# Performance work log

Measured on AMD Instinct MI355X. Metric: run time of the kernel, lower is better.

Reference implementation:

```python
import jax, jax.numpy as jnp
import numpy as np

D_MODEL = 1024
NUM_HEADS = 16
D_K = D_MODEL // NUM_HEADS
B, N = 2, 2048


def setup_inputs() -> dict:
    key = jax.random.key(0)
    ks = jax.random.split(key, 11)
    s = 1.0 / np.sqrt(D_MODEL)
    inp = {
        "query": jax.random.normal(ks[0], (B, N, D_MODEL), jnp.float32),
        "key": jax.random.normal(ks[1], (B, N, D_MODEL), jnp.float32),
        "value": jax.random.normal(ks[2], (B, N, D_MODEL), jnp.float32),
        "w_q": jax.random.normal(ks[3], (D_MODEL, D_MODEL), jnp.float32) * s,
        "b_q": jax.random.normal(ks[4], (D_MODEL,), jnp.float32) * s,
        "w_k": jax.random.normal(ks[5], (D_MODEL, D_MODEL), jnp.float32) * s,
        "b_k": jax.random.normal(ks[6], (D_MODEL,), jnp.float32) * s,
        "w_v": jax.random.normal(ks[7], (D_MODEL, D_MODEL), jnp.float32) * s,
        "b_v": jax.random.normal(ks[8], (D_MODEL,), jnp.float32) * s,
        "w_o": jax.random.normal(ks[9], (D_MODEL, D_MODEL), jnp.float32) * s,
        "b_o": jax.random.normal(ks[10], (D_MODEL,), jnp.float32) * s,
    }
    return inp


def reference(query, key, value, w_q, b_q, w_k, b_k, w_v, b_v, w_o, b_o):
    Bq, Nq, _ = query.shape
    # projections (torch Linear: x @ W.T + b)
    Q = (query @ w_q.T + b_q).reshape(Bq, Nq, NUM_HEADS, D_K).transpose(0, 2, 1, 3)
    K = (key @ w_k.T + b_k).reshape(Bq, -1, NUM_HEADS, D_K).transpose(0, 2, 1, 3)
    V = (value @ w_v.T + b_v).reshape(Bq, -1, NUM_HEADS, D_K).transpose(0, 2, 1, 3)
    scores = jnp.einsum("bhqd,bhkd->bhqk", Q, K) / np.sqrt(D_K).astype(np.float32)
    attn = jax.nn.softmax(scores, axis=-1)  # dropout p=0.0 -> identity
    ctx = jnp.einsum("bhqk,bhkd->bhqd", attn, V)
    ctx = ctx.transpose(0, 2, 1, 3).reshape(Bq, Nq, D_MODEL)
    return ctx @ w_o.T + b_o
```

## Files before the change

### kernel.cpp

```cpp
#include <hip/hip_runtime.h>
#include <math.h>

#define D_MODEL 1024
#define NUM_HEADS 16
#define DK 64
#define BATCH 2
#define NSEQ 2048
#define MROWS (BATCH * NSEQ)

typedef __attribute__((ext_vector_type(8))) short bf16x8;
typedef __attribute__((ext_vector_type(4))) short s16x4;
typedef __attribute__((ext_vector_type(4))) float f32x4;
typedef unsigned short u16;

static __device__ __forceinline__ u16 f2bf_rne(float x) {
    union { float f; unsigned u; } v; v.f = x;
    unsigned r = v.u + 0x7fffu + ((v.u >> 16) & 1u);
    return (u16)(r >> 16);
}
static __device__ __forceinline__ void split_bf16(float x, u16& hi, u16& lo) {
    union { float f; unsigned u; } v; v.f = x;
    unsigned hb = v.u & 0xffff0000u;
    hi = (u16)(hb >> 16);
    union { unsigned u; float f; } hv; hv.u = hb;
    lo = f2bf_rne(x - hv.f);
}

#define AS1 __attribute__((address_space(1)))
#define AS3 __attribute__((address_space(3)))
static __device__ __forceinline__ void gl_lds16(const void* g, void* l) {
    __builtin_amdgcn_global_load_lds((AS1 void*)(uintptr_t)g, (AS3 void*)l, 16, 0, 0);
}

struct SplitN { const float* src[4]; u16* h[4]; u16* l[4]; };
__global__ __launch_bounds__(256)
void split_multi(SplitN args, int n8)
{
    const int w = blockIdx.y;
    const int i = blockIdx.x * 256 + threadIdx.x;
    if (i >= n8) return;
    const float* src = args.src[w];
    float4 a = ((const float4*)src)[2 * i];
    float4 b = ((const float4*)src)[2 * i + 1];
    float x[8] = {a.x, a.y, a.z, a.w, b.x, b.y, b.z, b.w};
    u16 hh[8], ll[8];
#pragma unroll
    for (int j = 0; j < 8; ++j) split_bf16(x[j], hh[j], ll[j]);
    *(uint4*)(args.h[w] + 8 * (size_t)i) = *(uint4*)hh;
    *(uint4*)(args.l[w] + 8 * (size_t)i) = *(uint4*)ll;
}

#define GBM 128
#define GBN 64
#define GBK 64

struct GemmDesc {
    const u16 *Ah, *Al, *Wh, *Wl;
    const float* bias;
    float* outF;
    u16 *outH, *outL;
    float scale;
    int mode;
};
struct GemmBatch { GemmDesc d[3]; };

__global__ __launch_bounds__(256)
void gemm_mfma_batch(GemmBatch batch, int M, int N, int K)
{
    __shared__ u16 SM[2 * GBM * GBK + 2 * GBN * GBK];
    u16* As_h = SM;
    u16* As_l = SM + GBM * GBK;
    u16* Ws_h = SM + 2 * GBM * GBK;
    u16* Ws_l = SM + 2 * GBM * GBK + GBN * GBK;

    const GemmDesc d = batch.d[blockIdx.z];
    const int tid  = threadIdx.x;
    const int wv   = tid >> 6, lane = tid & 63;
    const int quad = lane >> 4, lcol = lane & 15;
    const int bm = blockIdx.x * GBM, bn = blockIdx.y * GBN;
    const int wm = (wv >> 1) * 64, wn = (wv & 1) * 32;
    const int sj = lane >> 3, sg = lane & 7;
    const int sgx8 = ((sg ^ sj) << 3);

    f32x4 acc[4][2];
#pragma unroll
    for (int i = 0; i < 4; ++i)
#pragma unroll
        for (int j = 0; j < 2; ++j) acc[i][j] = (f32x4){0.f, 0.f, 0.f, 0.f};

    for (int k0 = 0; k0 < K; k0 += GBK) {
        __syncthreads();
#pragma unroll
        for (int c = 0; c < 4; ++c) {
            const int r0 = wv * 32 + c * 8;
            gl_lds16(d.Ah + (size_t)(bm + r0 + sj) * K + k0 + sgx8, As_h + r0 * GBK);
            gl_lds16(d.Al + (size_t)(bm + r0 + sj) * K + k0 + sgx8, As_l + r0 * GBK);
        }
#pragma unroll
        for (int c = 0; c < 2; ++c) {
            const int r0 = wv * 16 + c * 8;
            gl_lds16(d.Wh + (size_t)(bn + r0 + sj) * K + k0 + sgx8, Ws_h + r0 * GBK);
            gl_lds16(d.Wl + (size_t)(bn + r0 + sj) * K + k0 + sgx8, Ws_l + r0 * GBK);
        }
        __syncthreads();

#pragma unroll
        for (int hf = 0; hf < 2; ++hf) {
            const int sl = ((((hf << 2) + quad) ^ (lcol & 7)) << 3);
            bf16x8 bh[2], bl[2];
#pragma unroll
            for (int j = 0; j < 2; ++j) {
                const int rn = wn + (j << 4) + lcol;
                bh[j] = *(const bf16x8*)(Ws_h + rn * GBK + sl);
                bl[j] = *(const bf16x8*)(Ws_l + rn * GBK + sl);
            }
#pragma unroll
            for (int i = 0; i < 4; ++i) {
                const int rm = wm + (i << 4) + lcol;
                bf16x8 ah = *(const bf16x8*)(As_h + rm * GBK + sl);
                bf16x8 al = *(const bf16x8*)(As_l + rm * GBK + sl);
#pragma unroll
                for (int j = 0; j < 2; ++j) {
                    acc[i][j] = __builtin_amdgcn_mfma_f32_16x16x32_bf16(ah, bh[j], acc[i][j], 0, 0, 0);
                    acc[i][j] = __builtin_amdgcn_mfma_f32_16x16x32_bf16(al, bh[j], acc[i][j], 0, 0, 0);
                    acc[i][j] = __builtin_amdgcn_mfma_f32_16x16x32_bf16(ah, bl[j], acc[i][j], 0, 0, 0);
                }
            }
        }
    }

    if (d.mode == 2) {
        const int TS = 136;
        u16* T = SM;
        __syncthreads();
#pragma unroll
        for (int j = 0; j < 2; ++j) {
            const int cl = wn + (j << 4) + lcol;
            const float bj = d.bias[bn + cl];
#pragma unroll
            for (int i = 0; i < 4; ++i) {
                const int r0 = wm + (i << 4) + quad * 4;
                u16 pk[4];
#pragma unroll
                for (int r = 0; r < 4; ++r) pk[r] = f2bf_rne(acc[i][j][r] + bj);
                *(ushort4*)(T + cl * TS + r0) = *(ushort4*)pk;
            }
        }
        __syncthreads();
        const int dd = tid >> 2, pt = tid & 3;
        const int bidx = bm >> 11, hh = bn >> 6;
        u16* dst = d.outH + ((size_t)(bidx * NUM_HEADS + hh) * DK + dd) * NSEQ
                 + (bm & (NSEQ - 1)) + pt * 32;
        const u16* src = T + dd * TS + pt * 32;
#pragma unroll
        for (int k = 0; k < 4; ++k)
            ((uint4*)dst)[k] = *(const uint4*)(src + 8 * k);
        return;
    }

#pragma unroll
    for (int j = 0; j < 2; ++j) {
        const int col = bn + wn + (j << 4) + lcol;
        const float bj = d.bias[col];
#pragma unroll
        for (int i = 0; i < 4; ++i) {
#pragma unroll
            for (int r = 0; r < 4; ++r) {
                const int row = bm + wm + (i << 4) + quad * 4 + r;
                const float v = (acc[i][j][r] + bj) * d.scale;
                const size_t o = (size_t)row * N + col;
                if (d.mode == 0) {
                    d.outF[o] = v;
                } else {
                    u16 hi, lo;
                    split_bf16(v, hi, lo);
                    d.outH[o] = hi;
                    d.outL[o] = lo;
                }
            }
        }
    }
}

__global__ __launch_bounds__(256)
void flash_attn(const u16* __restrict__ Qh_g, const u16* __restrict__ Ql_g,
                const u16* __restrict__ Kh_g, const u16* __restrict__ Kl_g,
                const u16* __restrict__ Vt_g,
                u16* __restrict__ Ch_g, u16* __restrict__ Cl_g)
{
    __shared__ __align__(16) u16 Ks_h[64][72], Ks_l[64][72];
    __shared__ __align__(16) u16 Vs[64][72];

    const int tid  = threadIdx.x;
    const int wv   = tid >> 6;
    const int lane = tid & 63;
    const int quad = lane >> 4;
    const int lcol = lane & 15;
    const int h    = blockIdx.x;
    const int q0   = blockIdx.y << 7;
    const int b    = blockIdx.z;
    const size_t hbase  = (size_t)b * NSEQ * D_MODEL + (size_t)h * DK;
    const size_t vtbase = (size_t)(b * NUM_HEADS + h) * DK * NSEQ;

    bf16x8 bQh[2][2], bQl[2][2];
#pragma unroll
    for (int s = 0; s < 2; ++s) {
        const u16* qh = Qh_g + hbase + (size_t)(q0 + wv * 32 + s * 16 + lcol) * D_MODEL;
        const u16* ql = Ql_g + hbase + (size_t)(q0 + wv * 32 + s * 16 + lcol) * D_MODEL;
#pragma unroll
        for (int c = 0; c < 2; ++c) {
            bQh[s][c] = *(const bf16x8*)(qh + c * 32 + quad * 8);
            bQl[s][c] = *(const bf16x8*)(ql + c * 32 + quad * 8);
        }
    }

    f32x4 Oacc[2][4];
#pragma unroll
    for (int s = 0; s < 2; ++s)
#pragma unroll
        for (int t = 0; t < 4; ++t) Oacc[s][t] = (f32x4){0.f, 0.f, 0.f, 0.f};
    float mrow[2] = {-INFINITY, -INFINITY};
    float lrow[2] = {0.f, 0.f};

    const int lr = tid >> 2;
    const int lc = (tid & 3) << 4;

    const int NT = NSEQ / 64;
    const u16* gKh = Kh_g + hbase + (size_t)lr * D_MODEL + lc;
    const u16* gKl = Kl_g + hbase + (size_t)lr * D_MODEL + lc;
    const u16* gV  = Vt_g + vtbase + (size_t)lr * NSEQ + lc;

    uint4 s0 = *(const uint4*)(gKh);
    uint4 s1 = *(const uint4*)(gKh + 8);
    uint4 s2 = *(const uint4*)(gKl);
    uint4 s3 = *(const uint4*)(gKl + 8);
    uint4 s4 = *(const uint4*)(gV);
    uint4 s5 = *(const uint4*)(gV + 8);

    for (int kt = 0; kt < NT; ++kt) {
        __syncthreads();
        *(uint4*)&Ks_h[lr][lc]     = s0;
        *(uint4*)&Ks_h[lr][lc + 8] = s1;
        *(uint4*)&Ks_l[lr][lc]     = s2;
        *(uint4*)&Ks_l[lr][lc + 8] = s3;
        *(uint4*)&Vs[lr][lc]       = s4;
        *(uint4*)&Vs[lr][lc + 8]   = s5;
        __syncthreads();
        if (kt + 1 < NT) {
            const size_t ko = (size_t)(kt + 1) << 6;
            s0 = *(const uint4*)(gKh + ko * D_MODEL);
            s1 = *(const uint4*)(gKh + ko * D_MODEL + 8);
            s2 = *(const uint4*)(gKl + ko * D_MODEL);
            s3 = *(const uint4*)(gKl + ko * D_MODEL + 8);
            s4 = *(const uint4*)(gV + ko);
            s5 = *(const uint4*)(gV + ko + 8);
        }

        f32x4 S[2][4];
        __builtin_amdgcn_s_setprio(1);
#pragma unroll
        for (int t = 0; t < 4; ++t) {
            bf16x8 aKh0 = *(const bf16x8*)&Ks_h[(t << 4) + lcol][quad * 8];
            bf16x8 aKh1 = *(const bf16x8*)&Ks_h[(t << 4) + lcol][32 + quad * 8];
            bf16x8 aKl0 = *(const bf16x8*)&Ks_l[(t << 4) + lcol][quad * 8];
            bf16x8 aKl1 = *(const bf16x8*)&Ks_l[(t << 4) + lcol][32 + quad * 8];
#pragma unroll
            for (int s = 0; s < 2; ++s) {
                f32x4 a = (f32x4){0.f, 0.f, 0.f, 0.f};
                a = __builtin_amdgcn_mfma_f32_16x16x32_bf16(aKh0, bQh[s][0], a, 0, 0, 0);
                a = __builtin_amdgcn_mfma_f32_16x16x32_bf16(aKh1, bQh[s][1], a, 0, 0, 0);
                a = __builtin_amdgcn_mfma_f32_16x16x32_bf16(aKl0, bQh[s][0], a, 0, 0, 0);
                a = __builtin_amdgcn_mfma_f32_16x16x32_bf16(aKl1, bQh[s][1], a, 0, 0, 0);
                a = __builtin_amdgcn_mfma_f32_16x16x32_bf16(aKh0, bQl[s][0], a, 0, 0, 0);
                a = __builtin_amdgcn_mfma_f32_16x16x32_bf16(aKh1, bQl[s][1], a, 0, 0, 0);
                S[s][t] = a;
            }
        }
        __builtin_amdgcn_s_setprio(0);

        bf16x8 pb[2][2];
#pragma unroll
        for (int s = 0; s < 2; ++s) {
            float m16 = -INFINITY;
#pragma unroll
            for (int t = 0; t < 4; ++t)
#pragma unroll
                for (int r = 0; r < 4; ++r) m16 = fmaxf(m16, S[s][t][r]);
            m16 = fmaxf(m16, __shfl_xor(m16, 16, 64));
            m16 = fmaxf(m16, __shfl_xor(m16, 32, 64));
            const float mn = fmaxf(mrow[s], m16);
            const float alpha = __expf(mrow[s] - mn);
            mrow[s] = mn;

            float p[4][4];
            float psum = 0.f;
#pragma unroll
            for (int t = 0; t < 4; ++t)
#pragma unroll
                for (int r = 0; r < 4; ++r) {
                    const float pv = __expf(S[s][t][r] - mn);
                    p[t][r] = pv;
                    psum += pv;
                }
            psum += __shfl_xor(psum, 16, 64);
            psum += __shfl_xor(psum, 32, 64);
            lrow[s] = alpha * lrow[s] + psum;

#pragma unroll
            for (int c = 0; c < 2; ++c) {
                bf16x8 v;
#pragma unroll
                for (int r = 0; r < 4; ++r) {
                    v[r]     = (short)f2bf_rne(p[2 * c][r]);
                    v[4 + r] = (short)f2bf_rne(p[2 * c + 1][r]);
                }
                pb[s][c] = v;
            }
#pragma unroll
            for (int t = 0; t < 4; ++t)
#pragma unroll
                for (int r = 0; r < 4; ++r) Oacc[s][t][r] *= alpha;
        }

        __builtin_amdgcn_s_setprio(1);
#pragma unroll
        for (int dt = 0; dt < 4; ++dt) {
            const u16* vr = &Vs[(dt << 4) + lcol][0];
#pragma unroll
            for (int c = 0; c < 2; ++c) {
                s16x4 alo = *(const s16x4*)(vr + c * 32 + quad * 4);
                s16x4 ahi = *(const s16x4*)(vr + c * 32 + 16 + quad * 4);
                bf16x8 aV;
#pragma unroll
                for (int r = 0; r < 4; ++r) { aV[r] = alo[r]; aV[4 + r] = ahi[r]; }
#pragma unroll
                for (int s = 0; s < 2; ++s)
                    Oacc[s][dt] = __builtin_amdgcn_mfma_f32_16x16x32_bf16(aV, pb[s][c], Oacc[s][dt], 0, 0, 0);
            }
        }
        __builtin_amdgcn_s_setprio(0);
    }

#pragma unroll
    for (int s = 0; s < 2; ++s) {
        const float inv = 1.f / lrow[s];
        const size_t base = hbase + (size_t)(q0 + wv * 32 + s * 16 + lcol) * D_MODEL;
#pragma unroll
        for (int dt = 0; dt < 4; ++dt) {
            u16 hv[4], lv[4];
#pragma unroll
            for (int r = 0; r < 4; ++r)
                split_bf16(Oacc[s][dt][r] * inv, hv[r], lv[r]);
            const size_t o = base + (dt << 4) + quad * 4;
            *(ushort4*)(Ch_g + o) = *(ushort4*)hv;
            *(ushort4*)(Cl_g + o) = *(ushort4*)lv;
        }
    }
}

extern "C" void kernel_launch(void* const* d_in, const int* in_sizes, int n_in,
                              void* d_out, int out_size, void* d_ws, size_t ws_size,
                              hipStream_t stream)
{
    const float* query = (const float*)d_in[0];
    const float* key_i = (const float*)d_in[1];
    const float* value = (const float*)d_in[2];
    const float* w_q   = (const float*)d_in[3];
    const float* b_q   = (const float*)d_in[4];
    const float* w_k   = (const float*)d_in[5];
    const float* b_k   = (const float*)d_in[6];
    const float* w_v   = (const float*)d_in[7];
    const float* b_v   = (const float*)d_in[8];
    const float* w_o   = (const float*)d_in[9];
    const float* b_o   = (const float*)d_in[10];
    float* out = (float*)d_out;

    const size_t WE = (size_t)D_MODEL * D_MODEL;
    const size_t AE = (size_t)MROWS * D_MODEL;

    u16* p = (u16*)d_ws;
    u16* Wqh = p;            u16* Wql = Wqh + WE;
    u16* Wkh = Wql + WE;     u16* Wkl = Wkh + WE;
    u16* Wvh = Wkl + WE;     u16* Wvl = Wvh + WE;
    u16* Woh = Wvl + WE;     u16* Wol = Woh + WE;
    u16* base = Wol + WE;

    SplitN ws4;
    ws4.src[0] = w_q; ws4.h[0] = Wqh; ws4.l[0] = Wql;
    ws4.src[1] = w_k; ws4.h[1] = Wkh; ws4.l[1] = Wkl;
    ws4.src[2] = w_v; ws4.h[2] = Wvh; ws4.l[2] = Wvl;
    ws4.src[3] = w_o; ws4.h[3] = Woh; ws4.l[3] = Wol;
    split_multi<<<dim3((unsigned)(WE / 8 / 256), 4), 256, 0, stream>>>(ws4, (int)(WE / 8));

    const float qscale = 0.125f;
    dim3 fgrid(NUM_HEADS, NSEQ / 128, BATCH);
    dim3 ggrid3(MROWS / GBM, D_MODEL / GBN, 3);
    dim3 ggrid1(MROWS / GBM, D_MODEL / GBN, 1);
    const int an8 = (int)(AE / 8);

    const size_t fused_bytes = 2 * (8 * WE + 11 * AE);
    if (ws_size >= fused_bytes) {
        u16* INqh = base;          u16* INql = INqh + AE;
        u16* INkh = INql + AE;     u16* INkl = INkh + AE;
        u16* INvh = INkl + AE;     u16* INvl = INvh + AE;
        u16* Qph  = INvl + AE;     u16* Qpl  = Qph + AE;
        u16* Kph  = Qpl + AE;      u16* Kpl  = Kph + AE;
        u16* VT   = Kpl + AE;
        u16* Ch   = INqh;          u16* Cl   = INql;

        SplitN as3;
        as3.src[0] = query; as3.h[0] = INqh; as3.l[0] = INql;
        as3.src[1] = key_i; as3.h[1] = INkh; as3.l[1] = INkl;
        as3.src[2] = value; as3.h[2] = INvh; as3.l[2] = INvl;
        as3.src[3] = query; as3.h[3] = INqh; as3.l[3] = INql;
        split_multi<<<dim3((unsigned)(AE / 8 / 256), 3), 256, 0, stream>>>(as3, an8);

        GemmBatch gb;
        gb.d[0] = {INqh, INql, Wqh, Wql, b_q, nullptr, Qph, Qpl, qscale, 1};
        gb.d[1] = {INkh, INkl, Wkh, Wkl, b_k, nullptr, Kph, Kpl, 1.0f,   1};
        gb.d[2] = {INvh, INvl, Wvh, Wvl, b_v, nullptr, VT,  nullptr, 1.0f, 2};
        gemm_mfma_batch<<<ggrid3, 256, 0, stream>>>(gb, MROWS, D_MODEL, D_MODEL);

        flash_attn<<<fgrid, 256, 0, stream>>>(Qph, Qpl, Kph, Kpl, VT, Ch, Cl);

        GemmBatch go;
        go.d[0] = {Ch, Cl, Woh, Wol, b_o, out, nullptr, nullptr, 1.0f, 0};
        gemm_mfma_batch<<<ggrid1, 256, 0, stream>>>(go, MROWS, D_MODEL, D_MODEL);
    } else {
        u16* INh = base;           u16* INl = INh + AE;
        u16* Qph = INl + AE;       u16* Qpl = Qph + AE;
        u16* Kph = Qpl + AE;       u16* Kpl = Kph + AE;
        u16* VT  = Kpl + AE;
        u16* Ch  = INh;            u16* Cl  = INl;

        SplitN s1;
        s1.src[0] = query; s1.h[0] = INh; s1.l[0] = INl;
        s1.src[1] = s1.src[2] = s1.src[3] = query;
        s1.h[1] = s1.h[2] = s1.h[3] = INh; s1.l[1] = s1.l[2] = s1.l[3] = INl;

        GemmBatch g;
        s1.src[0] = query;
        split_multi<<<dim3((unsigned)(AE / 8 / 256), 1), 256, 0, stream>>>(s1, an8);
        g.d[0] = {INh, INl, Wqh, Wql, b_q, nullptr, Qph, Qpl, qscale, 1};
        gemm_mfma_batch<<<ggrid1, 256, 0, stream>>>(g, MROWS, D_MODEL, D_MODEL);

        s1.src[0] = key_i;
        split_multi<<<dim3((unsigned)(AE / 8 / 256), 1), 256, 0, stream>>>(s1, an8);
        g.d[0] = {INh, INl, Wkh, Wkl, b_k, nullptr, Kph, Kpl, 1.0f, 1};
        gemm_mfma_batch<<<ggrid1, 256, 0, stream>>>(g, MROWS, D_MODEL, D_MODEL);

        s1.src[0] = value;
        split_multi<<<dim3((unsigned)(AE / 8 / 256), 1), 256, 0, stream>>>(s1, an8);
        g.d[0] = {INh, INl, Wvh, Wvl, b_v, nullptr, VT, nullptr, 1.0f, 2};
        gemm_mfma_batch<<<ggrid1, 256, 0, stream>>>(g, MROWS, D_MODEL, D_MODEL);

        flash_attn<<<fgrid, 256, 0, stream>>>(Qph, Qpl, Kph, Kpl, VT, Ch, Cl);

        g.d[0] = {Ch, Cl, Woh, Wol, b_o, out, nullptr, nullptr, 1.0f, 0};
        gemm_mfma_batch<<<ggrid1, 256, 0, stream>>>(g, MROWS, D_MODEL, D_MODEL);
    }
}
```

Baseline: 332.1 us.

## Halve flash-attention query tile to 64 rows and use packed bf16 conversion

Each flash-attention block now handles 64 query rows instead of 128, with each wave owning one 16-row slice, so the grid doubles to 1024 blocks and register pressure drops. The software round-to-nearest bf16 conversion of probabilities is replaced with the hardware v_cvt_pk_bf16_f32 instruction, and the row max is reduced via a three-input max pattern. The cost is that every K/V tile is now loaded twice as often per query row, doubling K/V traffic, and each block does less MFMA work to hide each barrier and load.

```diff
diff --git a/kernel.cpp b/kernel.cpp
--- a/kernel.cpp
+++ b/kernel.cpp
@@ -24,6 +24,14 @@
     hi = (u16)(hb >> 16);
     union { unsigned u; float f; } hv; hv.u = hb;
     lo = f2bf_rne(x - hv.f);
+}
+static __device__ __forceinline__ unsigned cvt_pk_bf16(float a, float b) {
+    unsigned w;
+    asm("v_cvt_pk_bf16_f32 %0, %1, %2" : "=v"(w) : "v"(a), "v"(b));
+    return w;
+}
+static __device__ __forceinline__ float max3f(float a, float b, float c) {
+    return fmaxf(fmaxf(a, b), c);
 }
 
 #define AS1 __attribute__((address_space(1)))
@@ -197,30 +205,27 @@
     const int quad = lane >> 4;
     const int lcol = lane & 15;
     const int h    = blockIdx.x;
-    const int q0   = blockIdx.y << 7;
+    const int q0   = blockIdx.y << 6;
     const int b    = blockIdx.z;
     const size_t hbase  = (size_t)b * NSEQ * D_MODEL + (size_t)h * DK;
     const size_t vtbase = (size_t)(b * NUM_HEADS + h) * DK * NSEQ;
 
-    bf16x8 bQh[2][2], bQl[2][2];
-#pragma unroll
-    for (int s = 0; s < 2; ++s) {
-        const u16* qh = Qh_g + hbase + (size_t)(q0 + wv * 32 + s * 16 + lcol) * D_MODEL;
-        const u16* ql = Ql_g + hbase + (size_t)(q0 + wv * 32 + s * 16 + lcol) * D_MODEL;
+    bf16x8 bQh[2], bQl[2];
+    {
+        const u16* qh = Qh_g + hbase + (size_t)(q0 + wv * 16 + lcol) * D_MODEL;
+        const u16* ql = Ql_g + hbase + (size_t)(q0 + wv * 16 + lcol) * D_MODEL;
 #pragma unroll
         for (int c = 0; c < 2; ++c) {
-            bQh[s][c] = *(const bf16x8*)(qh + c * 32 + quad * 8);
-            bQl[s][c] = *(const bf16x8*)(ql + c * 32 + quad * 8);
-        }
-    }
-
-    f32x4 Oacc[2][4];
-#pragma unroll
-    for (int s = 0; s < 2; ++s)
-#pragma unroll
-        for (int t = 0; t < 4; ++t) Oacc[s][t] = (f32x4){0.f, 0.f, 0.f, 0.f};
-    float mrow[2] = {-INFINITY, -INFINITY};
-    float lrow[2] = {0.f, 0.f};
+            bQh[c] = *(const bf16x8*)(qh + c * 32 + quad * 8);
+            bQl[c] = *(const bf16x8*)(ql + c * 32 + quad * 8);
+        }
+    }
+
+    f32x4 Oacc[4];
+#pragma unroll
+    for (int t = 0; t < 4; ++t) Oacc[t] = (f32x4){0.f, 0.f, 0.f, 0.f};
+    float mrow = -INFINITY;
+    float lrow = 0.f;
 
     const int lr = tid >> 2;
     const int lc = (tid & 3) << 4;
@@ -256,7 +261,7 @@
             s5 = *(const uint4*)(gV + ko + 8);
         }
 
-        f32x4 S[2][4];
+        f32x4 S[4];
         __builtin_amdgcn_s_setprio(1);
 #pragma unroll
         for (int t = 0; t < 4; ++t) {
@@ -264,33 +269,30 @@
             bf16x8 aKh1 = *(const bf16x8*)&Ks_h[(t << 4) + lcol][32 + quad * 8];
             bf16x8 aKl0 = *(const bf16x8*)&Ks_l[(t << 4) + lcol][quad * 8];
             bf16x8 aKl1 = *(const bf16x8*)&Ks_l[(t << 4) + lcol][32 + quad * 8];
-#pragma unroll
-            for (int s = 0; s < 2; ++s) {
-                f32x4 a = (f32x4){0.f, 0.f, 0.f, 0.f};
-                a = __builtin_amdgcn_mfma_f32_16x16x32_bf16(aKh0, bQh[s][0], a, 0, 0, 0);
-                a = __builtin_amdgcn_mfma_f32_16x16x32_bf16(aKh1, bQh[s][1], a, 0, 0, 0);
-                a = __builtin_amdgcn_mfma_f32_16x16x32_bf16(aKl0, bQh[s][0], a, 0, 0, 0);
-                a = __builtin_amdgcn_mfma_f32_16x16x32_bf16(aKl1, bQh[s][1], a, 0, 0, 0);
-                a = __builtin_amdgcn_mfma_f32_16x16x32_bf16(aKh0, bQl[s][0], a, 0, 0, 0);
-                a = __builtin_amdgcn_mfma_f32_16x16x32_bf16(aKh1, bQl[s][1], a, 0, 0, 0);
-                S[s][t] = a;
-            }
+            f32x4 a = (f32x4){0.f, 0.f, 0.f, 0.f};
+            a = __builtin_amdgcn_mfma_f32_16x16x32_bf16(aKh0, bQh[0], a, 0, 0, 0);
+            a = __builtin_amdgcn_mfma_f32_16x16x32_bf16(aKh1, bQh[1], a, 0, 0, 0);
+            a = __builtin_amdgcn_mfma_f32_16x16x32_bf16(aKl0, bQh[0], a, 0, 0, 0);
+            a = __builtin_amdgcn_mfma_f32_16x16x32_bf16(aKl1, bQh[1], a, 0, 0, 0);
+            a = __builtin_amdgcn_mfma_f32_16x16x32_bf16(aKh0, bQl[0], a, 0, 0, 0);
+            a = __builtin_amdgcn_mfma_f32_16x16x32_bf16(aKh1, bQl[1], a, 0, 0, 0);
+            S[t] = a;
         }
         __builtin_amdgcn_s_setprio(0);
 
-        bf16x8 pb[2][2];
-#pragma unroll
-        for (int s = 0; s < 2; ++s) {
-            float m16 = -INFINITY;
-#pragma unroll
-            for (int t = 0; t < 4; ++t)
-#pragma unroll
-                for (int r = 0; r < 4; ++r) m16 = fmaxf(m16, S[s][t][r]);
+        bf16x8 pb[2];
+        {
+            float m0 = max3f(S[0][0], S[0][1], S[0][2]);
+            float m1 = max3f(S[0][3], S[1][0], S[1][1]);
+            float m2 = max3f(S[1][2], S[1][3], S[2][0]);
+            float m3 = max3f(S[2][1], S[2][2], S[2][3]);
+            float m4 = max3f(S[3][0], S[3][1], S[3][2]);
+            float m16 = fmaxf(max3f(m0, m1, S[3][3]), fmaxf(m2, fmaxf(m3, m4)));
             m16 = fmaxf(m16, __shfl_xor(m16, 16, 64));
             m16 = fmaxf(m16, __shfl_xor(m16, 32, 64));
-            const float mn = fmaxf(mrow[s], m16);
-            const float alpha = __expf(mrow[s] - mn);
-            mrow[s] = mn;
+            const float mn = fmaxf(mrow, m16);
+            const float alpha = __expf(mrow - mn);
+            mrow = mn;
 
             float p[4][4];
             float psum = 0.f;
@@ -298,28 +300,30 @@
             for (int t = 0; t < 4; ++t)
 #pragma unroll
                 for (int r = 0; r < 4; ++r) {
-                    const float pv = __expf(S[s][t][r] - mn);
+                    const float pv = __expf(S[t][r] - mn);
                     p[t][r] = pv;
                     psum += pv;
                 }
             psum += __shfl_xor(psum, 16, 64);
             psum += __shfl_xor(psum, 32, 64);
-            lrow[s] = alpha * lrow[s] + psum;
-
-#pragma unroll
-            for (int c = 0; c < 2; ++c) {
-                bf16x8 v;
-#pragma unroll
-                for (int r = 0; r < 4; ++r) {
-                    v[r]     = (short)f2bf_rne(p[2 * c][r]);
-                    v[4 + r] = (short)f2bf_rne(p[2 * c + 1][r]);
-                }
-                pb[s][c] = v;
-            }
+            lrow = alpha * lrow + psum;
+
+            union { unsigned w[4]; bf16x8 v; } P0, P1;
+            P0.w[0] = cvt_pk_bf16(p[0][0], p[0][1]);
+            P0.w[1] = cvt_pk_bf16(p[0][2], p[0][3]);
+            P0.w[2] = cvt_pk_bf16(p[1][0], p[1][1]);
+            P0.w[3] = cvt_pk_bf16(p[1][2], p[1][3]);
+            P1.w[0] = cvt_pk_bf16(p[2][0], p[2][1]);
+            P1.w[1] = cvt_pk_bf16(p[2][2], p[2][3]);
+            P1.w[2] = cvt_pk_bf16(p[3][0], p[3][1]);
+            P1.w[3] = cvt_pk_bf16(p[3][2], p[3][3]);
+            pb[0] = P0.v;
+            pb[1] = P1.v;
+
 #pragma unroll
             for (int t = 0; t < 4; ++t)
 #pragma unroll
-                for (int r = 0; r < 4; ++r) Oacc[s][t][r] *= alpha;
+                for (int r = 0; r < 4; ++r) Oacc[t][r] *= alpha;
         }
 
         __builtin_amdgcn_s_setprio(1);
@@ -333,24 +337,21 @@
                 bf16x8 aV;
 #pragma unroll
                 for (int r = 0; r < 4; ++r) { aV[r] = alo[r]; aV[4 + r] = ahi[r]; }
-#pragma unroll
-                for (int s = 0; s < 2; ++s)
-                    Oacc[s][dt] = __builtin_amdgcn_mfma_f32_16x16x32_bf16(aV, pb[s][c], Oacc[s][dt], 0, 0, 0);
+                Oacc[dt] = __builtin_amdgcn_mfma_f32_16x16x32_bf16(aV, pb[c], Oacc[dt], 0, 0, 0);
             }
         }
         __builtin_amdgcn_s_setprio(0);
     }
 
-#pragma unroll
-    for (int s = 0; s < 2; ++s) {
-        const float inv = 1.f / lrow[s];
-        const size_t base = hbase + (size_t)(q0 + wv * 32 + s * 16 + lcol) * D_MODEL;
+    {
+        const float inv = 1.f / lrow;
+        const size_t base = hbase + (size_t)(q0 + wv * 16 + lcol) * D_MODEL;
 #pragma unroll
         for (int dt = 0; dt < 4; ++dt) {
             u16 hv[4], lv[4];
 #pragma unroll
             for (int r = 0; r < 4; ++r)
-                split_bf16(Oacc[s][dt][r] * inv, hv[r], lv[r]);
+                split_bf16(Oacc[dt][r] * inv, hv[r], lv[r]);
             const size_t o = base + (dt << 4) + quad * 4;
             *(ushort4*)(Ch_g + o) = *(ushort4*)hv;
             *(ushort4*)(Cl_g + o) = *(ushort4*)lv;
@@ -393,7 +394,7 @@
     split_multi<<<dim3((unsigned)(WE / 8 / 256), 4), 256, 0, stream>>>(ws4, (int)(WE / 8));
 
     const float qscale = 0.125f;
-    dim3 fgrid(NUM_HEADS, NSEQ / 128, BATCH);
+    dim3 fgrid(NUM_HEADS, NSEQ / 64, BATCH);
     dim3 ggrid3(MROWS / GBM, D_MODEL / GBN, 3);
     dim3 ggrid1(MROWS / GBM, D_MODEL / GBN, 1);
     const int an8 = (int)(AE / 8);
```

After: 345.3 us. 4.0% more time.

## Double-buffer K/V tiles in flash attention and use packed bf16 converts

Applied to the files above, without the earlier changes.

Double-buffers the K and V shared-memory tiles so the next tile is stored while the current one is consumed, cutting two barriers per iteration to one. Replaces the per-element software bf16 rounding of P with the hardware packed convert instruction and uses three-input max for the row max. The V^T projection output is permuted within 32-element groups so the V operand becomes a single 16-byte LDS read instead of two 8-byte reads plus shuffles. This doubles LDS use per block, which may lower occupancy, and relies on the permuted V layout being consistent across kernels.

```diff
diff --git a/kernel.cpp b/kernel.cpp
--- a/kernel.cpp
+++ b/kernel.cpp
@@ -24,6 +24,14 @@
     hi = (u16)(hb >> 16);
     union { unsigned u; float f; } hv; hv.u = hb;
     lo = f2bf_rne(x - hv.f);
+}
+static __device__ __forceinline__ unsigned cvt_pk_bf16(float a, float b) {
+    unsigned w;
+    asm("v_cvt_pk_bf16_f32 %0, %1, %2" : "=v"(w) : "v"(a), "v"(b));
+    return w;
+}
+static __device__ __forceinline__ float max3f(float a, float b, float c) {
+    return fmaxf(fmaxf(a, b), c);
 }
 
 #define AS1 __attribute__((address_space(1)))
@@ -153,8 +161,12 @@
                  + (bm & (NSEQ - 1)) + pt * 32;
         const u16* src = T + dd * TS + pt * 32;
 #pragma unroll
-        for (int k = 0; k < 4; ++k)
-            ((uint4*)dst)[k] = *(const uint4*)(src + 8 * k);
+        for (int u = 0; u < 4; ++u) {
+            ushort4 lo = *(const ushort4*)(src + 4 * u);
+            ushort4 hi = *(const ushort4*)(src + 16 + 4 * u);
+            u16 w[8] = {lo.x, lo.y, lo.z, lo.w, hi.x, hi.y, hi.z, hi.w};
+            ((uint4*)dst)[u] = *(uint4*)w;
+        }
         return;
     }
 
@@ -188,8 +200,8 @@
                 const u16* __restrict__ Vt_g,
                 u16* __restrict__ Ch_g, u16* __restrict__ Cl_g)
 {
-    __shared__ __align__(16) u16 Ks_h[64][72], Ks_l[64][72];
-    __shared__ __align__(16) u16 Vs[64][72];
+    __shared__ __align__(16) u16 Ks_h[2][64][72], Ks_l[2][64][72];
+    __shared__ __align__(16) u16 Vs[2][64][72];
 
     const int tid  = threadIdx.x;
     const int wv   = tid >> 6;
@@ -236,34 +248,34 @@
     uint4 s3 = *(const uint4*)(gKl + 8);
     uint4 s4 = *(const uint4*)(gV);
     uint4 s5 = *(const uint4*)(gV + 8);
+    *(uint4*)&Ks_h[0][lr][lc]     = s0;
+    *(uint4*)&Ks_h[0][lr][lc + 8] = s1;
+    *(uint4*)&Ks_l[0][lr][lc]     = s2;
+    *(uint4*)&Ks_l[0][lr][lc + 8] = s3;
+    *(uint4*)&Vs[0][lr][lc]       = s4;
+    *(uint4*)&Vs[0][lr][lc + 8]   = s5;
+    s0 = *(const uint4*)(gKh + (size_t)64 * D_MODEL);
+    s1 = *(const uint4*)(gKh + (size_t)64 * D_MODEL + 8);
+    s2 = *(const uint4*)(gKl + (size_t)64 * D_MODEL);
+    s3 = *(const uint4*)(gKl + (size_t)64 * D_MODEL + 8);
+    s4 = *(const uint4*)(gV + 64);
+    s5 = *(const uint4*)(gV + 64 + 8);
+    __syncthreads();
 
     for (int kt = 0; kt < NT; ++kt) {
-        __syncthreads();
-        *(uint4*)&Ks_h[lr][lc]     = s0;
-        *(uint4*)&Ks_h[lr][lc + 8] = s1;
-        *(uint4*)&Ks_l[lr][lc]     = s2;
-        *(uint4*)&Ks_l[lr][lc + 8] = s3;
-        *(uint4*)&Vs[lr][lc]       = s4;
-        *(uint4*)&Vs[lr][lc + 8]   = s5;
-        __syncthreads();
-        if (kt + 1 < NT) {
-            const size_t ko = (size_t)(kt + 1) << 6;
-            s0 = *(const uint4*)(gKh + ko * D_MODEL);
-            s1 = *(const uint4*)(gKh + ko * D_MODEL + 8);
-            s2 = *(const uint4*)(gKl + ko * D_MODEL);
-            s3 = *(const uint4*)(gKl + ko * D_MODEL + 8);
-            s4 = *(const uint4*)(gV + ko);
-            s5 = *(const uint4*)(gV + ko + 8);
-        }
+        const int cur = kt & 1;
+        const u16 (*Kh)[72] = Ks_h[cur];
+        const u16 (*Kl)[72] = Ks_l[cur];
+        const u16 (*Vv)[72] = Vs[cur];
 
         f32x4 S[2][4];
         __builtin_amdgcn_s_setprio(1);
 #pragma unroll
         for (int t = 0; t < 4; ++t) {
-            bf16x8 aKh0 = *(const bf16x8*)&Ks_h[(t << 4) + lcol][quad * 8];
-            bf16x8 aKh1 = *(const bf16x8*)&Ks_h[(t << 4) + lcol][32 + quad * 8];
-            bf16x8 aKl0 = *(const bf16x8*)&Ks_l[(t << 4) + lcol][quad * 8];
-            bf16x8 aKl1 = *(const bf16x8*)&Ks_l[(t << 4) + lcol][32 + quad * 8];
+            bf16x8 aKh0 = *(const bf16x8*)&Kh[(t << 4) + lcol][quad * 8];
+            bf16x8 aKh1 = *(const bf16x8*)&Kh[(t << 4) + lcol][32 + quad * 8];
+            bf16x8 aKl0 = *(const bf16x8*)&Kl[(t << 4) + lcol][quad * 8];
+            bf16x8 aKl1 = *(const bf16x8*)&Kl[(t << 4) + lcol][32 + quad * 8];
 #pragma unroll
             for (int s = 0; s < 2; ++s) {
                 f32x4 a = (f32x4){0.f, 0.f, 0.f, 0.f};
@@ -281,11 +293,12 @@
         bf16x8 pb[2][2];
 #pragma unroll
         for (int s = 0; s < 2; ++s) {
-            float m16 = -INFINITY;
-#pragma unroll
-            for (int t = 0; t < 4; ++t)
-#pragma unroll
-                for (int r = 0; r < 4; ++r) m16 = fmaxf(m16, S[s][t][r]);
+            float m0 = max3f(S[s][0][0], S[s][0][1], S[s][0][2]);
+            float m1 = max3f(S[s][0][3], S[s][1][0], S[s][1][1]);
+            float m2 = max3f(S[s][1][2], S[s][1][3], S[s][2][0]);
+            float m3 = max3f(S[s][2][1], S[s][2][2], S[s][2][3]);
+            float m4 = max3f(S[s][3][0], S[s][3][1], S[s][3][2]);
+            float m16 = fmaxf(max3f(m0, m1, S[s][3][3]), fmaxf(m2, fmaxf(m3, m4)));
             m16 = fmaxf(m16, __shfl_xor(m16, 16, 64));
             m16 = fmaxf(m16, __shfl_xor(m16, 32, 64));
             const float mn = fmaxf(mrow[s], m16);
@@ -306,39 +319,56 @@
             psum += __shfl_xor(psum, 32, 64);
             lrow[s] = alpha * lrow[s] + psum;
 
+            union { unsigned w[4]; bf16x8 v; } P0, P1;
+            P0.w[0] = cvt_pk_bf16(p[0][0], p[0][1]);
+            P0.w[1] = cvt_pk_bf16(p[0][2], p[0][3]);
+            P0.w[2] = cvt_pk_bf16(p[1][0], p[1][1]);
+            P0.w[3] = cvt_pk_bf16(p[1][2], p[1][3]);
+            P1.w[0] = cvt_pk_bf16(p[2][0], p[2][1]);
+            P1.w[1] = cvt_pk_bf16(p[2][2], p[2][3]);
+            P1.w[2] = cvt_pk_bf16(p[3][0], p[3][1]);
+            P1.w[3] = cvt_pk_bf16(p[3][2], p[3][3]);
+            pb[s][0] = P0.v;
+            pb[s][1] = P1.v;
+
+#pragma unroll
+            for (int t = 0; t < 4; ++t)
+#pragma unroll
+                for (int r = 0; r < 4; ++r) Oacc[s][t][r] *= alpha;
+        }
+
+        __builtin_amdgcn_s_setprio(1);
+#pragma unroll
+        for (int dt = 0; dt < 4; ++dt) {
+            const u16* vr = &Vv[(dt << 4) + lcol][0];
 #pragma unroll
             for (int c = 0; c < 2; ++c) {
-                bf16x8 v;
-#pragma unroll
-                for (int r = 0; r < 4; ++r) {
-                    v[r]     = (short)f2bf_rne(p[2 * c][r]);
-                    v[4 + r] = (short)f2bf_rne(p[2 * c + 1][r]);
-                }
-                pb[s][c] = v;
-            }
-#pragma unroll
-            for (int t = 0; t < 4; ++t)
-#pragma unroll
-                for (int r = 0; r < 4; ++r) Oacc[s][t][r] *= alpha;
-        }
-
-        __builtin_amdgcn_s_setprio(1);
-#pragma unroll
-        for (int dt = 0; dt < 4; ++dt) {
-            const u16* vr = &Vs[(dt << 4) + lcol][0];
-#pragma unroll
-            for (int c = 0; c < 2; ++c) {
-                s16x4 alo = *(const s16x4*)(vr + c * 32 + quad * 4);
-                s16x4 ahi = *(const s16x4*)(vr + c * 32 + 16 + quad * 4);
-                bf16x8 aV;
-#pragma unroll
-                for (int r = 0; r < 4; ++r) { aV[r] = alo[r]; aV[4 + r] = ahi[r]; }
+                bf16x8 aV = *(const bf16x8*)(vr + c * 32 + quad * 8);
 #pragma unroll
                 for (int s = 0; s < 2; ++s)
                     Oacc[s][dt] = __builtin_amdgcn_mfma_f32_16x16x32_bf16(aV, pb[s][c], Oacc[s][dt], 0, 0, 0);
             }
         }
         __builtin_amdgcn_s_setprio(0);
+
+        if (kt + 1 < NT) {
+            *(uint4*)&Ks_h[cur ^ 1][lr][lc]     = s0;
+            *(uint4*)&Ks_h[cur ^ 1][lr][lc + 8] = s1;
+            *(uint4*)&Ks_l[cur ^ 1][lr][lc]     = s2;
+            *(uint4*)&Ks_l[cur ^ 1][lr][lc + 8] = s3;
+            *(uint4*)&Vs[cur ^ 1][lr][lc]       = s4;
+            *(uint4*)&Vs[cur ^ 1][lr][lc + 8]   = s5;
+            if (kt + 2 < NT) {
+                const size_t ko = (size_t)(kt + 2) << 6;
+                s0 = *(const uint4*)(gKh + ko * D_MODEL);
+                s1 = *(const uint4*)(gKh + ko * D_MODEL + 8);
+                s2 = *(const uint4*)(gKl + ko * D_MODEL);
+                s3 = *(const uint4*)(gKl + ko * D_MODEL + 8);
+                s4 = *(const uint4*)(gV + ko);
+                s5 = *(const uint4*)(gV + ko + 8);
+            }
+        }
+        __syncthreads();
     }
 
 #pragma unroll
```

New measurement: 328.9 us. No clear change (-1.0%).
